# Kernel tuning notes

Hardware: AMD Instinct MI355X
Metric: run time of the kernel (lower is better)

## Reference

```python
import jax, jax.numpy as jnp
import numpy as np

N_ITEM_TYPE = 18
N_ITEM_FEAT = 11
N_TYPE_HIDDEN = 32
N_ITEM_HIDDEN = 128
BS, NA, NI = 32, 128, 128


def setup_inputs() -> dict:
    key = jax.random.key(0)
    k1, k2, k3, k4 = jax.random.split(key, 4)
    item_type = jax.random.randint(k1, (BS, NA, NI), 0, N_ITEM_TYPE, dtype=jnp.int64)
    item = jax.random.normal(k2, (BS, NA, NI, N_ITEM_FEAT), dtype=jnp.float32)
    emb = jax.random.normal(k3, (N_ITEM_TYPE, N_TYPE_HIDDEN), dtype=jnp.float32)
    W = jax.random.normal(k4, (N_TYPE_HIDDEN + N_ITEM_FEAT, N_ITEM_HIDDEN), dtype=jnp.float32) * 0.1
    b = jnp.zeros((N_ITEM_HIDDEN,), dtype=jnp.float32)
    return {"item_type": item_type, "item": item, "emb": emb, "W": W, "b": b}


def reference(item_type, item, emb, W, b):
    # embedding gather: [bs, na, ni, 32]
    h_type = emb[item_type]
    # concat features: [bs, na, ni, 43]
    h = jnp.concatenate([h_type, item], axis=-1)
    # Linear + ReLU: [bs, na, ni, n_item_hidden]
    h = jax.nn.relu(jnp.einsum("bnif,fh->bnih", h, W) + b)
    # max-pool over item axis: [bs, na, n_item_hidden]
    return jnp.max(h, axis=2)
```

## Files before the change

kernel.cpp:

```cpp
#include <hip/hip_runtime.h>
#include <hip/hip_bf16.h>
#include <stdint.h>
#include <float.h>


#define NITEM  128
#define NFEAT  11
#define NTH    32
#define NH     128
#define KREAL  43
#define KSTEPS 3
#define SLABDW (NITEM * NFEAT)

typedef __attribute__((ext_vector_type(8)))  _Float16 half8;
typedef __attribute__((ext_vector_type(2)))  __fp16   fp16x2;
typedef __attribute__((ext_vector_type(16))) float    f32x16;

union H8 { half8 h8; fp16x2 h2[4]; };

__global__ __launch_bounds__(64) void prep_b(const float* __restrict__ W,
                                             _Float16* __restrict__ Bpre) {
    const int frag = blockIdx.x;
    const int kk   = frag >> 2;
    const int n    = frag & 3;
    const int lane = threadIdx.x;
    const int col  = n * 32 + (lane & 31);
    const int k0   = kk * 16 + (lane >> 5) * 8;
    half8 pk;
    #pragma unroll
    for (int q = 0; q < 8; ++q) {
        const int k = k0 + q;
        pk[q] = (_Float16)((k < KREAL) ? W[k * NH + col] : 0.0f);
    }
    ((half8*)Bpre)[frag * 64 + lane] = pk;
}

__global__ __launch_bounds__(64, 2) void item_encoder(
    const int*      __restrict__ item_type,
    const float*    __restrict__ item,
    const float*    __restrict__ emb,
    const _Float16* __restrict__ Bpre,
    const float*    __restrict__ bias,
    float*          __restrict__ out)
{
    const int lane = threadIdx.x;
    const int l31  = lane & 31;
    const int lhi  = lane >> 5;
    const int bn   = blockIdx.x;

    half8 bf[KSTEPS][4];
    #pragma unroll
    for (int kk = 0; kk < KSTEPS; ++kk)
        #pragma unroll
        for (int n = 0; n < 4; ++n)
            bf[kk][n] = ((const half8*)Bpre)[(kk * 4 + n) * 64 + lane];

    int ty[4];
    {
        const int* tb = item_type + (size_t)bn * NITEM + l31;
        #pragma unroll
        for (int rb = 0; rb < 4; ++rb) ty[rb] = tb[rb * 32];
    }

    float bias4[4];
    #pragma unroll
    for (int n = 0; n < 4; ++n) bias4[n] = bias[n * 32 + l31];

    const float* feat = item + (size_t)bn * SLABDW;

    float vm[4] = { -FLT_MAX, -FLT_MAX, -FLT_MAX, -FLT_MAX };

    #pragma unroll
    for (int rb = 0; rb < 4; ++rb) {
        const int r = rb * 32 + l31;

        const float* eb = emb + ty[rb] * NTH + lhi * 8;
        const float4 e0 = *(const float4*)(eb);
        const float4 e1 = *(const float4*)(eb + 4);
        const float4 e2 = *(const float4*)(eb + 16);
        const float4 e3 = *(const float4*)(eb + 20);

        const float* fp = feat + r * NFEAT;
        float fv[8];
        #pragma unroll
        for (int q = 0; q < 8; ++q) {
            const int  f    = lhi ? ((q < 3) ? 8 + q : 10) : q;
            const bool dead = (lhi && q >= 3);
            const float x = fp[f];
            fv[q] = dead ? 0.0f : x;
        }

        H8 a0, a1, a2;
        a0.h2[0] = __builtin_amdgcn_cvt_pkrtz(e0.x, e0.y);
        a0.h2[1] = __builtin_amdgcn_cvt_pkrtz(e0.z, e0.w);
        a0.h2[2] = __builtin_amdgcn_cvt_pkrtz(e1.x, e1.y);
        a0.h2[3] = __builtin_amdgcn_cvt_pkrtz(e1.z, e1.w);
        a1.h2[0] = __builtin_amdgcn_cvt_pkrtz(e2.x, e2.y);
        a1.h2[1] = __builtin_amdgcn_cvt_pkrtz(e2.z, e2.w);
        a1.h2[2] = __builtin_amdgcn_cvt_pkrtz(e3.x, e3.y);
        a1.h2[3] = __builtin_amdgcn_cvt_pkrtz(e3.z, e3.w);
        a2.h2[0] = __builtin_amdgcn_cvt_pkrtz(fv[0], fv[1]);
        a2.h2[1] = __builtin_amdgcn_cvt_pkrtz(fv[2], fv[3]);
        a2.h2[2] = __builtin_amdgcn_cvt_pkrtz(fv[4], fv[5]);
        a2.h2[3] = __builtin_amdgcn_cvt_pkrtz(fv[6], fv[7]);

        f32x16 acc[4];
        #pragma unroll
        for (int n = 0; n < 4; ++n)
            #pragma unroll
            for (int rr = 0; rr < 16; ++rr) acc[n][rr] = 0.0f;

        #pragma unroll
        for (int n = 0; n < 4; ++n) acc[n] = __builtin_amdgcn_mfma_f32_32x32x16_f16(a0.h8, bf[0][n], acc[n], 0, 0, 0);
        #pragma unroll
        for (int n = 0; n < 4; ++n) acc[n] = __builtin_amdgcn_mfma_f32_32x32x16_f16(a1.h8, bf[1][n], acc[n], 0, 0, 0);
        #pragma unroll
        for (int n = 0; n < 4; ++n) acc[n] = __builtin_amdgcn_mfma_f32_32x32x16_f16(a2.h8, bf[2][n], acc[n], 0, 0, 0);

        #pragma unroll
        for (int n = 0; n < 4; ++n) {
            float m = acc[n][0];
            #pragma unroll
            for (int rr = 1; rr < 16; ++rr) m = fmaxf(m, acc[n][rr]);
            m = fmaxf(m, __shfl_xor(m, 32));
            vm[n] = fmaxf(vm[n], m);
        }
    }

    if (lane < 32) {
        #pragma unroll
        for (int n = 0; n < 4; ++n)
            out[(size_t)bn * NH + n * 32 + l31] = fmaxf(vm[n] + bias4[n], 0.0f);
    }
}

extern "C" void kernel_launch(void* const* d_in, const int* in_sizes, int n_in,
                              void* d_out, int out_size, void* d_ws, size_t ws_size,
                              hipStream_t stream) {
    const int*   item_type = (const int*)  d_in[0];
    const float* item      = (const float*)d_in[1];
    const float* emb       = (const float*)d_in[2];
    const float* W         = (const float*)d_in[3];
    const float* bias      = (const float*)d_in[4];
    float*       out       = (float*)d_out;
    _Float16*    Bpre      = (_Float16*)d_ws;

    prep_b<<<12, 64, 0, stream>>>(W, Bpre);
    item_encoder<<<32 * 128, 64, 0, stream>>>(item_type, item, emb, Bpre, bias, out);
}
```

Baseline: 93.97 us.

## Stage item slab in LDS, split N across two waves, pre-convert embeddings

Each block now uses two waves that split the 128 output columns, so each wave holds half the B fragments and accumulators. The per-row item features are loaded cooperatively into shared memory with coalesced float4 loads instead of strided scalar global loads. The embedding table is converted to fp16 once in the prep kernel, so each lane gathers one half8 per K step instead of float4 pairs plus conversions. This adds a __syncthreads and LDS reads, and both waves redundantly gather the type embeddings and item features.

```diff
diff --git a/kernel.cpp b/kernel.cpp
--- a/kernel.cpp
+++ b/kernel.cpp
@@ -11,6 +11,7 @@
 #define KREAL  43
 #define KSTEPS 3
 #define SLABDW (NITEM * NFEAT)
+#define EMBOFF (12 * 1024)
 
 typedef __attribute__((ext_vector_type(8)))  _Float16 half8;
 typedef __attribute__((ext_vector_type(2)))  __fp16   fp16x2;
@@ -18,42 +19,56 @@
 
 union H8 { half8 h8; fp16x2 h2[4]; };
 
-__global__ __launch_bounds__(64) void prep_b(const float* __restrict__ W,
-                                             _Float16* __restrict__ Bpre) {
-    const int frag = blockIdx.x;
-    const int kk   = frag >> 2;
-    const int n    = frag & 3;
+__global__ __launch_bounds__(64) void prep(const float* __restrict__ W,
+                                           const float* __restrict__ emb,
+                                           _Float16* __restrict__ ws) {
+    const int blk  = blockIdx.x;
     const int lane = threadIdx.x;
-    const int col  = n * 32 + (lane & 31);
-    const int k0   = kk * 16 + (lane >> 5) * 8;
-    half8 pk;
-    #pragma unroll
-    for (int q = 0; q < 8; ++q) {
-        const int k = k0 + q;
-        pk[q] = (_Float16)((k < KREAL) ? W[k * NH + col] : 0.0f);
+    if (blk < 12) {
+        const int kk  = blk >> 2;
+        const int n   = blk & 3;
+        const int col = n * 32 + (lane & 31);
+        const int k0  = kk * 16 + (lane >> 5) * 8;
+        half8 pk;
+        #pragma unroll
+        for (int q = 0; q < 8; ++q) {
+            const int k = k0 + q;
+            pk[q] = (_Float16)((k < KREAL) ? W[k * NH + col] : 0.0f);
+        }
+        ((half8*)ws)[blk * 64 + lane] = pk;
+    } else {
+        _Float16* eh = ws + EMBOFF / 2;
+        #pragma unroll
+        for (int j = 0; j < 9; ++j) {
+            const int idx = j * 64 + lane;
+            eh[idx] = (_Float16)emb[idx];
+        }
     }
-    ((half8*)Bpre)[frag * 64 + lane] = pk;
 }
 
-__global__ __launch_bounds__(64, 2) void item_encoder(
+__global__ __launch_bounds__(128, 4) void item_encoder(
     const int*      __restrict__ item_type,
     const float*    __restrict__ item,
-    const float*    __restrict__ emb,
-    const _Float16* __restrict__ Bpre,
+    const _Float16* __restrict__ ws,
     const float*    __restrict__ bias,
     float*          __restrict__ out)
 {
-    const int lane = threadIdx.x;
+    __shared__ float slab[SLABDW];
+
+    const int t    = threadIdx.x;
+    const int lane = t & 63;
+    const int w    = t >> 6;
     const int l31  = lane & 31;
     const int lhi  = lane >> 5;
     const int bn   = blockIdx.x;
 
-    half8 bf[KSTEPS][4];
-    #pragma unroll
-    for (int kk = 0; kk < KSTEPS; ++kk)
-        #pragma unroll
-        for (int n = 0; n < 4; ++n)
-            bf[kk][n] = ((const half8*)Bpre)[(kk * 4 + n) * 64 + lane];
+    {
+        const float4* gsl = (const float4*)(item + (size_t)bn * SLABDW);
+        float4*       lsl = (float4*)slab;
+        lsl[t]       = gsl[t];
+        lsl[t + 128] = gsl[t + 128];
+        if (t < 96) lsl[t + 256] = gsl[t + 256];
+    }
 
     int ty[4];
     {
@@ -62,75 +77,78 @@
         for (int rb = 0; rb < 4; ++rb) ty[rb] = tb[rb * 32];
     }
 
-    float bias4[4];
+    half8 bf[KSTEPS][2];
     #pragma unroll
-    for (int n = 0; n < 4; ++n) bias4[n] = bias[n * 32 + l31];
+    for (int kk = 0; kk < KSTEPS; ++kk)
+        #pragma unroll
+        for (int n2 = 0; n2 < 2; ++n2)
+            bf[kk][n2] = ((const half8*)ws)[(kk * 4 + (w * 2 + n2)) * 64 + lane];
 
-    const float* feat = item + (size_t)bn * SLABDW;
+    const _Float16* eh = ws + EMBOFF / 2;
+    half8 ea0[4], ea1[4];
+    #pragma unroll
+    for (int rb = 0; rb < 4; ++rb) {
+        const _Float16* eb = eh + ty[rb] * NTH + lhi * 8;
+        ea0[rb] = *(const half8*)(eb);
+        ea1[rb] = *(const half8*)(eb + 16);
+    }
 
-    float vm[4] = { -FLT_MAX, -FLT_MAX, -FLT_MAX, -FLT_MAX };
+    float bias2[2];
+    #pragma unroll
+    for (int n2 = 0; n2 < 2; ++n2) bias2[n2] = bias[(w * 2 + n2) * 32 + l31];
+
+    __syncthreads();
+
+    float vm[2] = { -FLT_MAX, -FLT_MAX };
 
     #pragma unroll
     for (int rb = 0; rb < 4; ++rb) {
         const int r = rb * 32 + l31;
 
-        const float* eb = emb + ty[rb] * NTH + lhi * 8;
-        const float4 e0 = *(const float4*)(eb);
-        const float4 e1 = *(const float4*)(eb + 4);
-        const float4 e2 = *(const float4*)(eb + 16);
-        const float4 e3 = *(const float4*)(eb + 20);
-
-        const float* fp = feat + r * NFEAT;
+        const float* sp = slab + r * NFEAT;
         float fv[8];
         #pragma unroll
         for (int q = 0; q < 8; ++q) {
             const int  f    = lhi ? ((q < 3) ? 8 + q : 10) : q;
             const bool dead = (lhi && q >= 3);
-            const float x = fp[f];
+            const float x = sp[f];
             fv[q] = dead ? 0.0f : x;
         }
 
-        H8 a0, a1, a2;
-        a0.h2[0] = __builtin_amdgcn_cvt_pkrtz(e0.x, e0.y);
-        a0.h2[1] = __builtin_amdgcn_cvt_pkrtz(e0.z, e0.w);
-        a0.h2[2] = __builtin_amdgcn_cvt_pkrtz(e1.x, e1.y);
-        a0.h2[3] = __builtin_amdgcn_cvt_pkrtz(e1.z, e1.w);
-        a1.h2[0] = __builtin_amdgcn_cvt_pkrtz(e2.x, e2.y);
-        a1.h2[1] = __builtin_amdgcn_cvt_pkrtz(e2.z, e2.w);
-        a1.h2[2] = __builtin_amdgcn_cvt_pkrtz(e3.x, e3.y);
-        a1.h2[3] = __builtin_amdgcn_cvt_pkrtz(e3.z, e3.w);
+        H8 a2;
         a2.h2[0] = __builtin_amdgcn_cvt_pkrtz(fv[0], fv[1]);
         a2.h2[1] = __builtin_amdgcn_cvt_pkrtz(fv[2], fv[3]);
         a2.h2[2] = __builtin_amdgcn_cvt_pkrtz(fv[4], fv[5]);
         a2.h2[3] = __builtin_amdgcn_cvt_pkrtz(fv[6], fv[7]);
 
-        f32x16 acc[4];
+        f32x16 acc[2];
         #pragma unroll
-        for (int n = 0; n < 4; ++n)
+        for (int n2 = 0; n2 < 2; ++n2)
             #pragma unroll
-            for (int rr = 0; rr < 16; ++rr) acc[n][rr] = 0.0f;
+            for (int rr = 0; rr < 16; ++rr) acc[n2][rr] = 0.0f;
 
         #pragma unroll
-        for (int n = 0; n < 4; ++n) acc[n] = __builtin_amdgcn_mfma_f32_32x32x16_f16(a0.h8, bf[0][n], acc[n], 0, 0, 0);
+        for (int n2 = 0; n2 < 2; ++n2) acc[n2] = __builtin_amdgcn_mfma_f32_32x32x16_f16(ea0[rb], bf[0][n2], acc[n2], 0, 0, 0);
         #pragma unroll
-        for (int n = 0; n < 4; ++n) acc[n] = __builtin_amdgcn_mfma_f32_32x32x16_f16(a1.h8, bf[1][n], acc[n], 0, 0, 0);
+        for (int n2 = 0; n2 < 2; ++n2) acc[n2] = __builtin_amdgcn_mfma_f32_32x32x16_f16(ea1[rb], bf[1][n2], acc[n2], 0, 0, 0);
         #pragma unroll
-        for (int n = 0; n < 4; ++n) acc[n] = __builtin_amdgcn_mfma_f32_32x32x16_f16(a2.h8, bf[2][n], acc[n], 0, 0, 0);
+        for (int n2 = 0; n2 < 2; ++n2) acc[n2] = __builtin_amdgcn_mfma_f32_32x32x16_f16(a2.h8,   bf[2][n2], acc[n2], 0, 0, 0);
 
         #pragma unroll
-        for (int n = 0; n < 4; ++n) {
-            float m = acc[n][0];
+        for (int n2 = 0; n2 < 2; ++n2) {
+            float m = acc[n2][0];
             #pragma unroll
-            for (int rr = 1; rr < 16; ++rr) m = fmaxf(m, acc[n][rr]);
+            for (int rr = 1; rr < 16; ++rr) m = fmaxf(m, acc[n2][rr]);
             m = fmaxf(m, __shfl_xor(m, 32));
-            vm[n] = fmaxf(vm[n], m);
+            vm[n2] = fmaxf(vm[n2], m);
         }
     }
 
     if (lane < 32) {
         #pragma unroll
-        for (int n = 0; n < 4; ++n)
-            out[(size_t)bn * NH + n * 32 + l31] = fmaxf(vm[n] + bias4[n], 0.0f);
+        for (int n2 = 0; n2 < 2; ++n2)
+            out[(size_t)bn * NH + (w * 2 + n2) * 32 + l31] =
+                fmaxf(vm[n2] + bias2[n2], 0.0f);
     }
 }
 
@@ -143,8 +161,8 @@
     const float* W         = (const float*)d_in[3];
     const float* bias      = (const float*)d_in[4];
     float*       out       = (float*)d_out;
-    _Float16*    Bpre      = (_Float16*)d_ws;
+    _Float16*    ws        = (_Float16*)d_ws;
 
-    prep_b<<<12, 64, 0, stream>>>(W, Bpre);
-    item_encoder<<<32 * 128, 64, 0, stream>>>(item_type, item, emb, Bpre, bias, out);
+    prep<<<13, 64, 0, stream>>>(W, emb, ws);
+    item_encoder<<<32 * 128, 128, 0, stream>>>(item_type, item, ws, bias, out);
 }
```

Result: faster. 88.12 us (-6.2%).
